# Optimization experiments

Measured on AMD Instinct MI355X. Metric: run time of the kernel, lower is better.

Reference implementation:

```python
import jax, jax.numpy as jnp
import numpy as np

N = 50000
E = 800000
IN_F = 128
OUT_F = 64
HEADS = 4
NEG_SLOPE = 0.2
EPS = 1e-8


def setup_inputs() -> dict:
    key = jax.random.key(0)
    k1, k2, k3, k4, k5 = jax.random.split(key, 5)
    x = jax.random.normal(k1, (N, IN_F), dtype=jnp.float32)
    edge_index = jax.random.randint(k2, (2, E), 0, N, dtype=jnp.int64)
    # xavier-uniform-like scales
    wb = float(np.sqrt(6.0 / (IN_F + OUT_F)))
    ab = float(np.sqrt(6.0 / (OUT_F + 1)))
    W = jax.random.uniform(k3, (HEADS, IN_F, OUT_F), dtype=jnp.float32, minval=-wb, maxval=wb)
    a_src = jax.random.uniform(k4, (HEADS, OUT_F, 1), dtype=jnp.float32, minval=-ab, maxval=ab)
    a_dst = jax.random.uniform(k5, (HEADS, OUT_F, 1), dtype=jnp.float32, minval=-ab, maxval=ab)
    return {"x": x, "edge_index": edge_index, "W": W, "a_src": a_src, "a_dst": a_dst}


def reference(x, edge_index, W, a_src, a_dst):
    n = x.shape[0]
    src, dst = edge_index[0], edge_index[1]
    # per-head projection: (H, N, F)
    Wh = jnp.einsum('ni,hif->hnf', x, W)
    e_src = jnp.einsum('hnf,hf->hn', Wh, a_src[..., 0])
    e_dst = jnp.einsum('hnf,hf->hn', Wh, a_dst[..., 0])
    e = jax.nn.leaky_relu(e_src[:, src] + e_dst[:, dst], NEG_SLOPE)  # (H, E)
    # edge softmax over destination; original initializes e_max to zeros,
    # so effective max is max(segment_max, 0)
    seg_max = jax.vmap(lambda eh: jax.ops.segment_max(eh, dst, num_segments=n))(e)
    e_max = jnp.maximum(seg_max, 0.0)
    exp_e = jnp.exp(e - e_max[:, dst])
    exp_sum = jax.vmap(lambda ee: jax.ops.segment_sum(ee, dst, num_segments=n))(exp_e)
    att = exp_e / (exp_sum[:, dst] + EPS)  # (H, E); dropout omitted (eval)
    # weighted scatter-add aggregation: (H, E, F) messages -> (H, N, F)
    msgs = att[..., None] * Wh[:, src]
    out = jax.vmap(lambda m: jax.ops.segment_sum(m, dst, num_segments=n))(msgs)
    # concat heads: (N, H*F)
    return out.transpose(1, 0, 2).reshape(n, -1)
```

## Files before the change

kernel.cpp:

```cpp
#include <hip/hip_runtime.h>
#include <hip/hip_bf16.h>

#define N_NODES 50000
#define E_EDGES 800000
#define IN_F    128
#define OUT_F   64
#define HEADS   4
#define HF      (HEADS * OUT_F)
#define NEG_SLOPE 0.2f
#define EPS     1e-8f
#define CAP     64
#define NB_INIT ((N_NODES + 255) / 256)

typedef __attribute__((ext_vector_type(8))) short bf16x8;
typedef __attribute__((ext_vector_type(4))) float f32x4;

__device__ __forceinline__ unsigned short f2bf(float f) {
    return __hip_bfloat16_raw(__float2bfloat16(f)).x;
}
__device__ __forceinline__ float bf2f(unsigned short u) {
    return __uint_as_float((unsigned)u << 16);
}

__global__ __launch_bounds__(256) void wcvt_kernel(
    const float* __restrict__ W,
    short* __restrict__ Wtb,
    int* __restrict__ cnt)
{
    const int i = blockIdx.x * 256 + threadIdx.x;
    if (i < N_NODES) {
        const int4 z = {0, 0, 0, 0};
        int4* p = (int4*)(cnt + i * 16);
        p[0] = z; p[1] = z; p[2] = z; p[3] = z;
    }
    if (i < HEADS * IN_F * OUT_F) {
        const int h  = i >> 13;
        const int fl = (i >> 7) & 63;
        const int k  = i & 127;
        Wtb[i] = (short)f2bf(W[h * (IN_F * OUT_F) + k * OUT_F + fl]);
    }
}

__global__ __launch_bounds__(256) void proj_kernel(
    const float* __restrict__ x,
    const short* __restrict__ Wtb,
    const float* __restrict__ a_src,
    const float* __restrict__ a_dst,
    const int* __restrict__ src,
    const int* __restrict__ dst,
    unsigned short* __restrict__ Whb,
    float* __restrict__ esrc,
    float* __restrict__ edst,
    int* __restrict__ cnt,
    unsigned short* __restrict__ csr)
{
    __shared__ short xs[16][136];
    __shared__ unsigned short ot[4][16][72];

    const int tid = threadIdx.x;
    const int n0 = blockIdx.x * 16;

    const int e  = blockIdx.x * 256 + tid;
    const int de = dst[e];
    const int se = src[e];

    {
        const int row = tid >> 4;
        const int kb = (tid & 15) * 8;
        const float* xp = x + (size_t)(n0 + row) * IN_F + kb;
        const float4 x0 = *(const float4*)(xp);
        const float4 x1 = *(const float4*)(xp + 4);
        bf16x8 v;
        v[0] = (short)f2bf(x0.x); v[1] = (short)f2bf(x0.y);
        v[2] = (short)f2bf(x0.z); v[3] = (short)f2bf(x0.w);
        v[4] = (short)f2bf(x1.x); v[5] = (short)f2bf(x1.y);
        v[6] = (short)f2bf(x1.z); v[7] = (short)f2bf(x1.w);
        *(bf16x8*)&xs[row][kb] = v;
    }
    __syncthreads();

    const int pos = atomicAdd(&cnt[de << 4], 1);

    const int h = tid >> 6;
    const int lane = tid & 63;
    const int c = lane & 15;
    const int quad = lane >> 4;

    bf16x8 a[4];
#pragma unroll
    for (int ks = 0; ks < 4; ++ks)
        a[ks] = *(const bf16x8*)&xs[c][ks * 32 + quad * 8];

    f32x4 acc[4];
#pragma unroll
    for (int nt = 0; nt < 4; ++nt) acc[nt] = (f32x4){0.f, 0.f, 0.f, 0.f};

    const short* Wh_head = Wtb + (h << 13);
#pragma unroll
    for (int nt = 0; nt < 4; ++nt) {
        const short* wrow = Wh_head + ((nt * 16 + c) << 7) + (quad << 3);
#pragma unroll
        for (int ks = 0; ks < 4; ++ks) {
            const bf16x8 b = *(const bf16x8*)(wrow + (ks << 5));
            acc[nt] = __builtin_amdgcn_mfma_f32_16x16x32_bf16(a[ks], b, acc[nt], 0, 0, 0);
        }
    }

    float ps[4] = {0.f, 0.f, 0.f, 0.f};
    float pd[4] = {0.f, 0.f, 0.f, 0.f};
#pragma unroll
    for (int nt = 0; nt < 4; ++nt) {
        const float as = a_src[h * OUT_F + nt * 16 + c];
        const float ad = a_dst[h * OUT_F + nt * 16 + c];
#pragma unroll
        for (int r = 0; r < 4; ++r) {
            ps[r] += acc[nt][r] * as;
            pd[r] += acc[nt][r] * ad;
        }
    }
#pragma unroll
    for (int m = 1; m < 16; m <<= 1) {
#pragma unroll
        for (int r = 0; r < 4; ++r) {
            ps[r] += __shfl_xor(ps[r], m);
            pd[r] += __shfl_xor(pd[r], m);
        }
    }
    if (c == 0) {
#pragma unroll
        for (int r = 0; r < 4; ++r) {
            const int n = n0 + quad * 4 + r;
            esrc[n * HEADS + h] = ps[r];
            edst[n * HEADS + h] = pd[r];
        }
    }

#pragma unroll
    for (int nt = 0; nt < 4; ++nt) {
#pragma unroll
        for (int r = 0; r < 4; ++r)
            ot[h][quad * 4 + r][nt * 16 + c] = f2bf(acc[nt][r]);
    }
    {
        const int row = lane >> 2;
        const int co  = (lane & 3) * 16;
        unsigned short* gp = Whb + (size_t)(n0 + row) * HF + h * OUT_F + co;
        const unsigned short* sp = &ot[h][row][co];
        *(int4*)(gp)     = *(const int4*)(sp);
        *(int4*)(gp + 8) = *(const int4*)(sp + 8);
    }

    if (pos < CAP)
        __builtin_nontemporal_store((unsigned short)se, &csr[(size_t)de * CAP + pos]);
}

__global__ __launch_bounds__(256) void aggregate_kernel(
    const int* __restrict__ cnt,
    const unsigned short* __restrict__ csr,
    const float* __restrict__ esrc,
    const float* __restrict__ edst,
    const unsigned short* __restrict__ Whb,
    float* __restrict__ out)
{
    __shared__ int   sb[4][64];
    __shared__ float pb[4][64][4];

    const int wid = threadIdx.x >> 6;
    const int lane = threadIdx.x & 63;
    const int d = blockIdx.x * 4 + wid;

    int deg = cnt[d << 4];
    deg = deg > CAP ? CAP : deg;

    const float4 ed4 = *(const float4*)(edst + d * HEADS);
    const int h = lane >> 4;
    const unsigned short* wbase = Whb + (lane << 2);

    float l0 = 0.f, l1 = 0.f, l2 = 0.f, l3 = 0.f;
    int sfill = 0;
    float4 pfill = {0.f, 0.f, 0.f, 0.f};
    if (lane < deg) {
        const int s = (int)__builtin_nontemporal_load(&csr[(size_t)d * CAP + lane]);
        const float4 es4 = *(const float4*)(esrc + s * HEADS);
        float v0 = es4.x + ed4.x; v0 = v0 > 0.f ? v0 : NEG_SLOPE * v0;
        float v1 = es4.y + ed4.y; v1 = v1 > 0.f ? v1 : NEG_SLOPE * v1;
        float v2 = es4.z + ed4.z; v2 = v2 > 0.f ? v2 : NEG_SLOPE * v2;
        float v3 = es4.w + ed4.w; v3 = v3 > 0.f ? v3 : NEG_SLOPE * v3;
        l0 = __expf(v0); l1 = __expf(v1); l2 = __expf(v2); l3 = __expf(v3);
        sfill = s;
        pfill = (float4){l0, l1, l2, l3};
    }
    sb[wid][lane] = sfill;
    *(float4*)pb[wid][lane] = pfill;

    float o0 = 0.f, o1 = 0.f, o2 = 0.f, o3 = 0.f;
    for (int i = 0; i < deg; i += 16) {
        int s[16];
#pragma unroll
        for (int j = 0; j < 16; ++j) s[j] = sb[wid][i + j];
        ushort4 w[16];
#pragma unroll
        for (int j = 0; j < 16; ++j)
            w[j] = *(const ushort4*)(wbase + (unsigned)s[j] * HF);
        float q[16];
#pragma unroll
        for (int j = 0; j < 16; ++j) q[j] = pb[wid][i + j][h];
#pragma unroll
        for (int j = 0; j < 16; ++j) {
            o0 += q[j] * bf2f(w[j].x);
            o1 += q[j] * bf2f(w[j].y);
            o2 += q[j] * bf2f(w[j].z);
            o3 += q[j] * bf2f(w[j].w);
        }
    }

#pragma unroll
    for (int m = 1; m < 64; m <<= 1) {
        l0 += __shfl_xor(l0, m);
        l1 += __shfl_xor(l1, m);
        l2 += __shfl_xor(l2, m);
        l3 += __shfl_xor(l3, m);
    }
    const float lsum = (h == 0) ? l0 : (h == 1) ? l1 : (h == 2) ? l2 : l3;
    const float r = 1.f / (lsum + EPS);

    const f32x4 o4 = {o0 * r, o1 * r, o2 * r, o3 * r};
    __builtin_nontemporal_store(o4, (f32x4*)(out + (size_t)d * HF + (lane << 2)));
}

extern "C" void kernel_launch(void* const* d_in, const int* in_sizes, int n_in,
                              void* d_out, int out_size, void* d_ws, size_t ws_size,
                              hipStream_t stream) {
    const float* x      = (const float*)d_in[0];
    const int*   eidx   = (const int*)d_in[1];
    const float* W      = (const float*)d_in[2];
    const float* a_src  = (const float*)d_in[3];
    const float* a_dst  = (const float*)d_in[4];
    float* out = (float*)d_out;

    const int* src = eidx;
    const int* dst = eidx + E_EDGES;

    unsigned short* Whb = (unsigned short*)d_ws;
    float* esrc   = (float*)(Whb + (size_t)N_NODES * HF);
    float* edst   = esrc + (size_t)N_NODES * HEADS;
    int*   cnt    = (int*)(edst + (size_t)N_NODES * HEADS);
    unsigned short* csr = (unsigned short*)(cnt + (size_t)N_NODES * 16);
    short* Wtb    = (short*)(csr + (size_t)N_NODES * CAP);

    wcvt_kernel<<<NB_INIT, 256, 0, stream>>>(W, Wtb, cnt);

    proj_kernel<<<N_NODES / 16, 256, 0, stream>>>(x, Wtb, a_src, a_dst, src, dst,
                                                  Whb, esrc, edst, cnt, csr);

    aggregate_kernel<<<N_NODES / 4, 256, 0, stream>>>(cnt, csr, esrc, edst, Whb, out);
}
```

Before: 193.8 us.

## Slice Wh into per-feature-slice planes and split aggregation across eight slice blocks

Stores the bf16 projected features as eight column slices of 32 features, each a contiguous plane over all nodes. The aggregation grid becomes eight times larger, with each block handling one slice for four destination nodes. The aim is a working set per slice that fits in cache and higher parallelism for the gather. The degree counters also lose their 64-byte padding, so same-line atomics can contend. The cost is eight-fold recomputation of the csr and esrc loads and exp per node, plus gathers of only 64 bytes per source row.

After: 269.8 us. +39.2%, slower.

```diff
diff --git a/kernel.cpp b/kernel.cpp
--- a/kernel.cpp
+++ b/kernel.cpp
@@ -10,10 +10,12 @@
 #define NEG_SLOPE 0.2f
 #define EPS     1e-8f
 #define CAP     64
+#define SLICE_F 32
 #define NB_INIT ((N_NODES + 255) / 256)
 
 typedef __attribute__((ext_vector_type(8))) short bf16x8;
 typedef __attribute__((ext_vector_type(4))) float f32x4;
+typedef __attribute__((ext_vector_type(2))) float f32x2;
 
 __device__ __forceinline__ unsigned short f2bf(float f) {
     return __hip_bfloat16_raw(__float2bfloat16(f)).x;
@@ -28,11 +30,7 @@
     int* __restrict__ cnt)
 {
     const int i = blockIdx.x * 256 + threadIdx.x;
-    if (i < N_NODES) {
-        const int4 z = {0, 0, 0, 0};
-        int4* p = (int4*)(cnt + i * 16);
-        p[0] = z; p[1] = z; p[2] = z; p[3] = z;
-    }
+    if (i < N_NODES) cnt[i] = 0;
     if (i < HEADS * IN_F * OUT_F) {
         const int h  = i >> 13;
         const int fl = (i >> 7) & 63;
@@ -79,7 +77,7 @@
     }
     __syncthreads();
 
-    const int pos = atomicAdd(&cnt[de << 4], 1);
+    const int pos = atomicAdd(&cnt[de], 1);
 
     const int h = tid >> 6;
     const int lane = tid & 63;
@@ -144,7 +142,8 @@
     {
         const int row = lane >> 2;
         const int co  = (lane & 3) * 16;
-        unsigned short* gp = Whb + (size_t)(n0 + row) * HF + h * OUT_F + co;
+        const int sl  = (h << 1) + (co >> 5);
+        unsigned short* gp = Whb + ((size_t)sl * N_NODES + (n0 + row)) * SLICE_F + (co & 31);
         const unsigned short* sp = &ot[h][row][co];
         *(int4*)(gp)     = *(const int4*)(sp);
         *(int4*)(gp + 8) = *(const int4*)(sp + 8);
@@ -162,70 +161,58 @@
     const unsigned short* __restrict__ Whb,
     float* __restrict__ out)
 {
-    __shared__ int   sb[4][64];
-    __shared__ float pb[4][64][4];
-
-    const int wid = threadIdx.x >> 6;
+    __shared__ unsigned short ssb[4][64];
+    __shared__ float spb[4][64];
+
+    const int wid  = threadIdx.x >> 6;
     const int lane = threadIdx.x & 63;
-    const int d = blockIdx.x * 4 + wid;
-
-    int deg = cnt[d << 4];
+    const int p = blockIdx.x & 7;
+    const int h = p >> 1;
+    const int d = (blockIdx.x >> 3) * 4 + wid;
+
+    int deg = cnt[d];
     deg = deg > CAP ? CAP : deg;
 
-    const float4 ed4 = *(const float4*)(edst + d * HEADS);
-    const int h = lane >> 4;
-    const unsigned short* wbase = Whb + (lane << 2);
-
-    float l0 = 0.f, l1 = 0.f, l2 = 0.f, l3 = 0.f;
-    int sfill = 0;
-    float4 pfill = {0.f, 0.f, 0.f, 0.f};
+    const float edh = edst[d * HEADS + h];
+
+    float lsum = 0.f;
+    unsigned short sfill = 0;
+    float pfill = 0.f;
     if (lane < deg) {
-        const int s = (int)__builtin_nontemporal_load(&csr[(size_t)d * CAP + lane]);
-        const float4 es4 = *(const float4*)(esrc + s * HEADS);
-        float v0 = es4.x + ed4.x; v0 = v0 > 0.f ? v0 : NEG_SLOPE * v0;
-        float v1 = es4.y + ed4.y; v1 = v1 > 0.f ? v1 : NEG_SLOPE * v1;
-        float v2 = es4.z + ed4.z; v2 = v2 > 0.f ? v2 : NEG_SLOPE * v2;
-        float v3 = es4.w + ed4.w; v3 = v3 > 0.f ? v3 : NEG_SLOPE * v3;
-        l0 = __expf(v0); l1 = __expf(v1); l2 = __expf(v2); l3 = __expf(v3);
-        sfill = s;
-        pfill = (float4){l0, l1, l2, l3};
-    }
-    sb[wid][lane] = sfill;
-    *(float4*)pb[wid][lane] = pfill;
-
-    float o0 = 0.f, o1 = 0.f, o2 = 0.f, o3 = 0.f;
-    for (int i = 0; i < deg; i += 16) {
-        int s[16];
-#pragma unroll
-        for (int j = 0; j < 16; ++j) s[j] = sb[wid][i + j];
-        ushort4 w[16];
-#pragma unroll
-        for (int j = 0; j < 16; ++j)
-            w[j] = *(const ushort4*)(wbase + (unsigned)s[j] * HF);
-        float q[16];
-#pragma unroll
-        for (int j = 0; j < 16; ++j) q[j] = pb[wid][i + j][h];
-#pragma unroll
-        for (int j = 0; j < 16; ++j) {
-            o0 += q[j] * bf2f(w[j].x);
-            o1 += q[j] * bf2f(w[j].y);
-            o2 += q[j] * bf2f(w[j].z);
-            o3 += q[j] * bf2f(w[j].w);
-        }
-    }
-
-#pragma unroll
-    for (int m = 1; m < 64; m <<= 1) {
-        l0 += __shfl_xor(l0, m);
-        l1 += __shfl_xor(l1, m);
-        l2 += __shfl_xor(l2, m);
-        l3 += __shfl_xor(l3, m);
-    }
-    const float lsum = (h == 0) ? l0 : (h == 1) ? l1 : (h == 2) ? l2 : l3;
+        const int s = (int)csr[(size_t)d * CAP + lane];
+        float v = esrc[s * HEADS + h] + edh;
+        v = v > 0.f ? v : NEG_SLOPE * v;
+        pfill = __expf(v);
+        lsum = pfill;
+        sfill = (unsigned short)s;
+    }
+    ssb[wid][lane] = sfill;
+    spb[wid][lane] = pfill;
+
+    const unsigned short* wslice =
+        Whb + (size_t)p * N_NODES * SLICE_F + ((lane & 15) << 1);
+    const int j0 = lane >> 4;
+
+    float a0 = 0.f, a1 = 0.f;
+#pragma unroll 4
+    for (int i = 0; i < deg; i += 4) {
+        const int   s = (int)ssb[wid][i + j0];
+        const float q = spb[wid][i + j0];
+        const ushort2 w = *(const ushort2*)(wslice + (unsigned)s * SLICE_F);
+        a0 += q * bf2f(w.x);
+        a1 += q * bf2f(w.y);
+    }
+    a0 += __shfl_xor(a0, 16); a0 += __shfl_xor(a0, 32);
+    a1 += __shfl_xor(a1, 16); a1 += __shfl_xor(a1, 32);
+#pragma unroll
+    for (int m = 1; m < 64; m <<= 1) lsum += __shfl_xor(lsum, m);
     const float r = 1.f / (lsum + EPS);
 
-    const f32x4 o4 = {o0 * r, o1 * r, o2 * r, o3 * r};
-    __builtin_nontemporal_store(o4, (f32x4*)(out + (size_t)d * HF + (lane << 2)));
+    if (lane < 16) {
+        const f32x2 o2 = {a0 * r, a1 * r};
+        float* op = out + (size_t)d * HF + (h << 6) + ((p & 1) << 5) + (lane << 1);
+        __builtin_nontemporal_store(o2, (f32x2*)op);
+    }
 }
 
 extern "C" void kernel_launch(void* const* d_in, const int* in_sizes, int n_in,
@@ -242,10 +229,10 @@
     const int* dst = eidx + E_EDGES;
 
     unsigned short* Whb = (unsigned short*)d_ws;
-    float* esrc   = (float*)(Whb + (size_t)N_NODES * HF);
+    float* esrc   = (float*)(Whb + (size_t)8 * N_NODES * SLICE_F);
     float* edst   = esrc + (size_t)N_NODES * HEADS;
     int*   cnt    = (int*)(edst + (size_t)N_NODES * HEADS);
-    unsigned short* csr = (unsigned short*)(cnt + (size_t)N_NODES * 16);
+    unsigned short* csr = (unsigned short*)(cnt + N_NODES);
     short* Wtb    = (short*)(csr + (size_t)N_NODES * CAP);
 
     wcvt_kernel<<<NB_INIT, 256, 0, stream>>>(W, Wtb, cnt);
@@ -253,5 +240,5 @@
     proj_kernel<<<N_NODES / 16, 256, 0, stream>>>(x, Wtb, a_src, a_dst, src, dst,
                                                   Whb, esrc, edst, cnt, csr);
 
-    aggregate_kernel<<<N_NODES / 4, 256, 0, stream>>>(cnt, csr, esrc, edst, Whb, out);
-}
+    aggregate_kernel<<<(N_NODES / 4) * 8, 256, 0, stream>>>(cnt, csr, esrc, edst, Whb, out);
+}
```
